# Kernel tuning notes

Hardware: AMD Instinct MI355X
Metric: run time of the kernel (lower is better)

Reference implementation:

```python
import jax, jax.numpy as jnp
import numpy as np

N_Q = 8
DIM = 2 ** N_Q          # 256
DEGREE = 3
ANSATZ_LAYERS = 2


def gelu(x):
    return jax.nn.gelu(x, approximate=False)


def layer_norm(x, g, b, eps=1e-5):
    mu = x.mean(-1, keepdims=True)
    v = x.var(-1, keepdims=True)
    return (x - mu) / jnp.sqrt(v + eps) * g + b


def apply_ry(state, theta, w, n):
    # state: (B, 2^n) complex64, theta: (B,) per-element angle
    half = theta * 0.5
    c, s = jnp.cos(half), jnp.sin(half)
    U = jnp.stack([jnp.stack([c, -s], -1), jnp.stack([s, c], -1)], -2).astype(state.dtype)
    L, R = 2 ** w, 2 ** (n - 1 - w)
    st = state.reshape(-1, L, 2, R)
    st = jnp.einsum('bij,bljr->blir', U, st)
    return st.reshape(state.shape)


def apply_crx(state, theta, c, t, n):
    # controlled-RX(theta), control wire c, target wire t (batched angles)
    half = theta * 0.5
    cs = jnp.cos(half).astype(state.dtype)
    ms = (-1j) * jnp.sin(half).astype(state.dtype)
    Rx = jnp.stack([jnp.stack([cs, ms], -1), jnp.stack([ms, cs], -1)], -2)  # (B,2,2)
    a, b = min(c, t), max(c, t)
    A, M, R = 2 ** a, 2 ** (b - a - 1), 2 ** (n - 1 - b)
    st = state.reshape(-1, A, 2, M, 2, R)
    if c < t:
        sub = st[:, :, 1]                              # control bit = 1 slice, (B,A,M,2,R)
        sub = jnp.einsum('bij,bamjr->bamir', Rx, sub)
        st = st.at[:, :, 1].set(sub)
    else:
        sub = st[:, :, :, :, 1]                        # (B,A,2,M,R)
        sub = jnp.einsum('bij,bajmr->baimr', Rx, sub)
        st = st.at[:, :, :, :, 1].set(sub)
    return st.reshape(state.shape)


def sim14(state, params, n, layers):
    # Sim et al. 2019 circuit 14: RY layer, CRX ring, RY layer, reversed CRX ring (4n params/layer)
    idx = 0
    for _ in range(layers):
        for q in range(n):
            state = apply_ry(state, params[:, idx + q], q, n)
        idx += n
        for q in range(n):
            state = apply_crx(state, params[:, idx + q], q, (q + 1) % n, n)
        idx += n
        for q in range(n):
            state = apply_ry(state, params[:, idx + q], q, n)
        idx += n
        for q in range(n):
            state = apply_crx(state, params[:, idx + q], q, (q - 1) % n, n)
        idx += n
    return state


def pauli_expvals(psi, n):
    # [<X_0..X_{n-1}>, <Y_0..>, <Z_0..>] for batched pure states psi: (B, 2^n)
    xs, ys, zs = [], [], []
    for w in range(n):
        L, R = 2 ** w, 2 ** (n - 1 - w)
        s = psi.reshape(-1, L, 2, R)
        s0, s1 = s[:, :, 0], s[:, :, 1]
        cross = (jnp.conj(s0) * s1).sum((1, 2))
        xs.append(2.0 * jnp.real(cross))
        ys.append(2.0 * jnp.imag(cross))
        zs.append((jnp.abs(s0) ** 2 - jnp.abs(s1) ** 2).sum((1, 2)))
    return jnp.stack(xs + ys + zs, axis=1).astype(jnp.float32)


def dwsep_conv(x, dw_w, dw_b, pw_w, pw_b, gn_g, gn_b, dilation):
    # depthwise-separable conv1d + GroupNorm(8) + GELU; x: (B, C, T)
    k = dw_w.shape[-1]
    pad = (k - 1) * dilation // 2
    y = jax.lax.conv_general_dilated(
        x, dw_w, window_strides=(1,), padding=[(pad, pad)], rhs_dilation=(dilation,),
        feature_group_count=x.shape[1], dimension_numbers=('NCH', 'OIH', 'NCH'))
    y = y + dw_b[None, :, None]
    y = jnp.einsum('oc,bct->bot', pw_w, y) + pw_b[None, :, None]
    B, C, T = y.shape
    g = y.reshape(B, 8, C // 8, T)
    mu = g.mean((2, 3), keepdims=True)
    var = g.var((2, 3), keepdims=True)
    y = ((g - mu) / jnp.sqrt(var + 1e-5)).reshape(B, C, T)
    return gelu(y * gn_g[None, :, None] + gn_b[None, :, None])


def setup_inputs() -> dict:
    key = jax.random.key(0)
    ks = iter(jax.random.split(key, 64))
    rn = lambda *s: jax.random.normal(next(ks), s, jnp.float32) * 0.05
    ru = lambda *s: jax.random.uniform(next(ks), s, dtype=jnp.float32)
    inp = dict(
        x=jax.random.normal(next(ks), (16, 363, 180), jnp.float32),
        net_w=rn(12, 15, 8), net_b=rn(12, 8),
        dwa_w=rn(96, 1, 7), dwa_b=rn(96), pwa_w=rn(96, 96), pwa_b=rn(96),
        gna_g=jnp.ones(96, jnp.float32), gna_b=jnp.zeros(96, jnp.float32),
        dwb_w=rn(96, 1, 7), dwb_b=rn(96), pwb_w=rn(96, 96), pwb_b=rn(96),
        gnb_g=jnp.ones(96, jnp.float32), gnb_b=jnp.zeros(96, jnp.float32),
        dwc_w=rn(96, 1, 7), dwc_b=rn(96), pwc_w=rn(96, 96), pwc_b=rn(96),
        gnc_g=jnp.ones(96, jnp.float32), gnc_b=jnp.zeros(96, jnp.float32),
        merge_w=rn(288, 128), merge_b=rn(128),
        merge_ln_g=jnp.ones(128, jnp.float32), merge_ln_b=jnp.zeros(128, jnp.float32),
        qproj_w=rn(128, 64), qproj_b=rn(64),
        poly_coeffs=ru(4), qff_params=ru(32),
        mix_re=ru(363), mix_im=ru(363),
        qout_w=rn(24, 128), qout_b=rn(128),
        fc_w=rn(78, 64), fc_b=rn(64),
        fus1_w=rn(192, 128), fus1_b=rn(128),
        fus_ln_g=jnp.ones(128, jnp.float32), fus_ln_b=jnp.zeros(128, jnp.float32),
        fus2_w=rn(128, 64), fus2_b=rn(64),
    )
    return inp


def reference(x, net_w, net_b, dwa_w, dwa_b, pwa_w, pwa_b, gna_g, gna_b,
              dwb_w, dwb_b, pwb_w, pwb_b, gnb_g, gnb_b,
              dwc_w, dwc_b, pwc_w, pwc_b, gnc_g, gnc_b,
              merge_w, merge_b, merge_ln_g, merge_ln_b,
              qproj_w, qproj_b, poly_coeffs, qff_params, mix_re, mix_im,
              qout_w, qout_b, fc_w, fc_b,
              fus1_w, fus1_b, fus_ln_g, fus_ln_b, fus2_w, fus2_b):
    B, T, C = x.shape
    # --- network projection: 12 contiguous networks of 15 ROIs -> d_net=8 each ---
    h = jnp.einsum('btki,kid->btkd', x.reshape(B, T, 12, 15), net_w) + net_b
    h = gelu(h).reshape(B, T, 96)
    # --- multiscale depthwise-separable convs ---
    ht = h.transpose(0, 2, 1)  # (B,96,T)
    a = dwsep_conv(ht, dwa_w, dwa_b, pwa_w, pwa_b, gna_g, gna_b, 1)
    b = dwsep_conv(ht, dwb_w, dwb_b, pwb_w, pwb_b, gnb_g, gnb_b, 4)
    c = dwsep_conv(ht, dwc_w, dwc_b, pwc_w, pwc_b, gnc_g, gnc_b, 16)
    cat = jnp.concatenate([a, b, c], axis=1).transpose(0, 2, 1)  # (B,T,288)
    h = gelu(layer_norm(cat @ merge_w + merge_b, merge_ln_g, merge_ln_b))  # (B,T,128)
    # --- QSVT quantum temporal mixing ---
    tp = jax.nn.sigmoid(h @ qproj_w + qproj_b) * (2.0 * np.pi)  # (B,T,64) rotation angles
    tp = tp.reshape(B * T, -1)
    base = jnp.zeros((B * T, DIM), jnp.complex64).at[:, 0].set(1.0)
    pc = poly_coeffs.astype(jnp.complex64)
    state = base
    acc = pc[0] * base
    for d in range(1, DEGREE + 1):
        state = sim14(state, tp, N_Q, ANSATZ_LAYERS)
        acc = acc + pc[d] * state
    acc = acc.reshape(B, T, DIM)
    mix = (mix_re + 1j * mix_im).astype(jnp.complex64)[:T]
    mixed = jnp.einsum('t,btd->bd', mix, acc)           # temporal mixing
    norm = jnp.linalg.norm(mixed, axis=1, keepdims=True)
    psi = mixed / (norm + 1e-9)
    psi = sim14(psi, jnp.broadcast_to(qff_params[None, :], (B, qff_params.shape[0])), N_Q, 1)
    exps = pauli_expvals(psi, N_Q)                      # (B,24)
    temporal = exps @ qout_w + qout_b                   # (B,128)
    # --- FC fingerprint ---
    xm = x - x.mean(1, keepdims=True)
    std = jnp.maximum(jnp.std(x, axis=1, keepdims=True, ddof=1), 1e-8)
    xn = xm / std
    corr = jnp.einsum('btc,btd->bcd', xn, xn) / (T - 1)
    bm = corr.reshape(B, 12, 15, 12, 15).mean((2, 4))   # (B,12,12) network-block means
    iu0, iu1 = jnp.triu_indices(12)
    fc_vec = bm[:, iu0, iu1]                            # (B,78)
    fc = gelu(fc_vec @ fc_w + fc_b)                     # (B,64)
    # --- fusion ---
    fused = jnp.concatenate([temporal, fc], axis=1)
    out = gelu(layer_norm(fused @ fus1_w + fus1_b, fus_ln_g, fus_ln_b)) @ fus2_w + fus2_b
    return out  # (B,64)
```

## Files before the change

kernel.cpp:

```cpp
#include <hip/hip_runtime.h>
#include <math.h>

#define NB 16
#define NT 363
#define NC 180
#define SZF 557568
#define NROW 5808

__device__ __forceinline__ float gelu_f(float x) {
  return 0.5f * x * (1.0f + erff(x * 0.7071067811865475244f));
}


template<int CTRL>
__device__ __forceinline__ float dppf(float x) {
  return __int_as_float(__builtin_amdgcn_update_dpp(
      0, __float_as_int(x), CTRL, 0xF, 0xF, true));
}

template<int LB>
__device__ __forceinline__ float lx(float x) {
  if constexpr (LB == 0) return dppf<0xB1>(x);
  else if constexpr (LB == 1) return dppf<0x4E>(x);
  else if constexpr (LB == 2) return __shfl_xor(x, 4);
  else if constexpr (LB == 3) return __shfl_xor(x, 8);
  else return __shfl_xor(x, 16);
}

template<int P>
__device__ __forceinline__ void ry_local8(float* re, float* im, float c, float s) {
#pragma unroll
  for (int j = 0; j < 8; ++j) {
    if ((j & (1 << P)) == 0) {
      int k = j | (1 << P);
      float r0 = re[j], i0 = im[j], r1 = re[k], i1 = im[k];
      re[j] = fmaf(c, r0, -s * r1); im[j] = fmaf(c, i0, -s * i1);
      re[k] = fmaf(s, r0,  c * r1); im[k] = fmaf(s, i0,  c * i1);
    }
  }
}

template<int LB>
__device__ __forceinline__ void ry_lane8(float* re, float* im, float c, float s, int lane) {
  float sg = (lane & (1 << LB)) ? s : -s;
#pragma unroll
  for (int j = 0; j < 8; ++j) {
    float br = lx<LB>(re[j]);
    float bi = lx<LB>(im[j]);
    re[j] = fmaf(c, re[j], sg * br);
    im[j] = fmaf(c, im[j], sg * bi);
  }
}

template<int Q, int P>
__device__ __forceinline__ void crx_ll8(float* re, float* im, float cs, float sn) {
#pragma unroll
  for (int j = 0; j < 8; ++j) {
    if ((j & (1 << Q)) && !(j & (1 << P))) {
      int k = j | (1 << P);
      float r0 = re[j], i0 = im[j], r1 = re[k], i1 = im[k];
      re[j] = fmaf(cs, r0,  sn * i1); im[j] = fmaf(cs, i0, -sn * r1);
      re[k] = fmaf(cs, r1,  sn * i0); im[k] = fmaf(cs, i1, -sn * r0);
    }
  }
}

template<int LBQ, int P>
__device__ __forceinline__ void crx_nl8(float* re, float* im, float cs, float sn, int lane) {
  if (lane & (1 << LBQ)) {
#pragma unroll
    for (int j = 0; j < 8; ++j) {
      if ((j & (1 << P)) == 0) {
        int k = j | (1 << P);
        float r0 = re[j], i0 = im[j], r1 = re[k], i1 = im[k];
        re[j] = fmaf(cs, r0,  sn * i1); im[j] = fmaf(cs, i0, -sn * r1);
        re[k] = fmaf(cs, r1,  sn * i0); im[k] = fmaf(cs, i1, -sn * r0);
      }
    }
  }
}

template<int Q, int LBP>
__device__ __forceinline__ void crx_ln8(float* re, float* im, float cs, float sn) {
#pragma unroll
  for (int j = 0; j < 8; ++j) {
    if (j & (1 << Q)) {
      float br = lx<LBP>(re[j]);
      float bi = lx<LBP>(im[j]);
      re[j] = fmaf(cs, re[j],  sn * bi);
      im[j] = fmaf(cs, im[j], -sn * br);
    }
  }
}

template<int LBQ, int LBP>
__device__ __forceinline__ void crx_nn8(float* re, float* im, float cs, float sn, int lane) {
  bool ctl = (lane & (1 << LBQ)) != 0;
#pragma unroll
  for (int j = 0; j < 8; ++j) {
    float br = lx<LBP>(re[j]);
    float bi = lx<LBP>(im[j]);
    if (ctl) {
      re[j] = fmaf(cs, re[j],  sn * bi);
      im[j] = fmaf(cs, im[j], -sn * br);
    }
  }
}

__device__ __forceinline__ void qlayer8(float* re, float* im,
                                        const float2* ang, int lane) {
  float2 a;
  a = ang[0];  ry_lane8<4>(re, im, a.x, a.y, lane);
  a = ang[1];  ry_lane8<3>(re, im, a.x, a.y, lane);
  a = ang[2];  ry_lane8<2>(re, im, a.x, a.y, lane);
  a = ang[3];  ry_lane8<1>(re, im, a.x, a.y, lane);
  a = ang[4];  ry_lane8<0>(re, im, a.x, a.y, lane);
  a = ang[5];  ry_local8<2>(re, im, a.x, a.y);
  a = ang[6];  ry_local8<1>(re, im, a.x, a.y);
  a = ang[7];  ry_local8<0>(re, im, a.x, a.y);
  a = ang[8];  crx_nn8<4, 3>(re, im, a.x, a.y, lane);
  a = ang[9];  crx_nn8<3, 2>(re, im, a.x, a.y, lane);
  a = ang[10]; crx_nn8<2, 1>(re, im, a.x, a.y, lane);
  a = ang[11]; crx_nn8<1, 0>(re, im, a.x, a.y, lane);
  a = ang[12]; crx_nl8<0, 2>(re, im, a.x, a.y, lane);
  a = ang[13]; crx_ll8<2, 1>(re, im, a.x, a.y);
  a = ang[14]; crx_ll8<1, 0>(re, im, a.x, a.y);
  a = ang[15]; crx_ln8<0, 4>(re, im, a.x, a.y);
  a = ang[16]; ry_lane8<4>(re, im, a.x, a.y, lane);
  a = ang[17]; ry_lane8<3>(re, im, a.x, a.y, lane);
  a = ang[18]; ry_lane8<2>(re, im, a.x, a.y, lane);
  a = ang[19]; ry_lane8<1>(re, im, a.x, a.y, lane);
  a = ang[20]; ry_lane8<0>(re, im, a.x, a.y, lane);
  a = ang[21]; ry_local8<2>(re, im, a.x, a.y);
  a = ang[22]; ry_local8<1>(re, im, a.x, a.y);
  a = ang[23]; ry_local8<0>(re, im, a.x, a.y);
  a = ang[24]; crx_nl8<4, 0>(re, im, a.x, a.y, lane);
  a = ang[25]; crx_nn8<3, 4>(re, im, a.x, a.y, lane);
  a = ang[26]; crx_nn8<2, 3>(re, im, a.x, a.y, lane);
  a = ang[27]; crx_nn8<1, 2>(re, im, a.x, a.y, lane);
  a = ang[28]; crx_nn8<0, 1>(re, im, a.x, a.y, lane);
  a = ang[29]; crx_ln8<2, 0>(re, im, a.x, a.y);
  a = ang[30]; crx_ll8<1, 2>(re, im, a.x, a.y);
  a = ang[31]; crx_ll8<0, 1>(re, im, a.x, a.y);
}

template<int P>
__device__ __forceinline__ void ryg(float* re, float* im, float c, float s, int lane) {
  if constexpr (P >= 2) {
    constexpr int mask = 1 << (P - 2);
    float sg = ((lane >> (P - 2)) & 1) ? s : -s;
#pragma unroll
    for (int j = 0; j < 4; ++j) {
      float br = __shfl_xor(re[j], mask);
      float bi = __shfl_xor(im[j], mask);
      re[j] = fmaf(c, re[j], sg * br);
      im[j] = fmaf(c, im[j], sg * bi);
    }
  } else {
#pragma unroll
    for (int k = 0; k < 2; ++k) {
      const int a = (P == 0) ? 2 * k : k;
      const int b = (P == 0) ? a + 1 : a + 2;
      float r0 = re[a], i0 = im[a], r1 = re[b], i1 = im[b];
      re[a] = fmaf(c, r0, -s * r1); im[a] = fmaf(c, i0, -s * i1);
      re[b] = fmaf(s, r0,  c * r1); im[b] = fmaf(s, i0,  c * i1);
    }
  }
}

template<int PC, int PT>
__device__ __forceinline__ void crxg(float* re, float* im, float cs, float sn, int lane) {
  if constexpr (PT >= 2) {
    constexpr int mask = 1 << (PT - 2);
#pragma unroll
    for (int j = 0; j < 4; ++j) {
      float br = __shfl_xor(re[j], mask);
      float bi = __shfl_xor(im[j], mask);
      bool ctrl;
      if constexpr (PC >= 2) ctrl = ((lane >> (PC - 2)) & 1) != 0;
      else                   ctrl = ((j >> PC) & 1) != 0;
      if (ctrl) {
        float nr = fmaf(cs, re[j],  sn * bi);
        float ni = fmaf(cs, im[j], -sn * br);
        re[j] = nr; im[j] = ni;
      }
    }
  } else {
#pragma unroll
    for (int k = 0; k < 2; ++k) {
      const int a = (PT == 0) ? 2 * k : k;
      const int b = (PT == 0) ? a + 1 : a + 2;
      bool ctrl;
      if constexpr (PC >= 2) ctrl = ((lane >> (PC - 2)) & 1) != 0;
      else                   ctrl = ((a >> PC) & 1) != 0;
      if (ctrl) {
        float r0 = re[a], i0 = im[a], r1 = re[b], i1 = im[b];
// ... 34 lines not shown
    int z = i / 56, r = i % 56, d = r / 7, k = r % 7;
    const float* w = (z == 0) ? wa : ((z == 1) ? wb : wc);
    wL[z][d][k] = w[(kg * 8 + d) * 7 + k];
  }
  for (int i = tid; i < 24; i += 256) {
    int z = i / 8, d = i % 8;
    const float* bias = (z == 0) ? ba : ((z == 1) ? bb : bc);
    bL[z][d] = bias[kg * 8 + d];
  }
  for (int i = tid; i < NT * 15; i += 256) {
    int t = i / 15, u = i % 15;
    xs[i] = x[((size_t)b * NT + t) * NC + kg * 15 + u];
  }
  __syncthreads();
  for (int i = tid; i < 8 * NT; i += 256) {
    int t = i % NT, d = i / NT;
    float acc2 = nbL[d];
#pragma unroll
    for (int u = 0; u < 15; ++u) acc2 = fmaf(xs[t * 15 + u], nwL[u * 8 + d], acc2);
    hrow[d][t] = gelu_f(acc2);
  }
  __syncthreads();
  for (int i = tid; i < 8 * NT; i += 256) {
    int t = i % NT, d = i / NT;
    int c = kg * 8 + d;
    float a0 = bL[0][d], a1 = bL[1][d], a2 = bL[2][d];
#pragma unroll
    for (int k = 0; k < 7; ++k) {
      int i1 = t + (k - 3);
      int i4 = t + (k - 3) * 4;
      int i16 = t + (k - 3) * 16;
      if (i1 >= 0 && i1 < NT)  a0 = fmaf(hrow[d][i1],  wL[0][d][k], a0);
      if (i4 >= 0 && i4 < NT)  a1 = fmaf(hrow[d][i4],  wL[1][d][k], a1);
      if (i16 >= 0 && i16 < NT) a2 = fmaf(hrow[d][i16], wL[2][d][k], a2);
    }
    size_t base = ((size_t)b * 96 + c) * NT + t;
    y1base[base] = a0;
    y1base[SZF + base] = a1;
    y1base[2 * SZF + base] = a2;
  }
}

__global__ __launch_bounds__(256) void k_pw(const float* __restrict__ y1base,
    const float* __restrict__ wA, const float* __restrict__ wB, const float* __restrict__ wC,
    const float* __restrict__ bA, const float* __restrict__ bB, const float* __restrict__ bC,
    float* __restrict__ y2base) {
  int b = blockIdx.x, tile = blockIdx.y, z = blockIdx.z, tid = threadIdx.x;
  const float* pw_w = (z == 0) ? wA : ((z == 1) ? wB : wC);
  const float* pw_b = (z == 0) ? bA : ((z == 1) ? bB : bC);
  const float* y1 = y1base + (size_t)z * SZF;
  float* y2 = y2base + (size_t)z * SZF;
  int t0 = tile * 64;
  __shared__ float y1t[96 * 64];
  __shared__ float pwL[96 * 97];
  for (int i = tid; i < 96 * 96; i += 256) {
    int o = i / 96, cc = i % 96;
    pwL[o * 97 + cc] = pw_w[i];
  }
  for (int i = tid; i < 96 * 64; i += 256) {
    int cc = i >> 6, t = i & 63;
    int tt = t0 + t;
    y1t[i] = (tt < NT) ? y1[(b * 96 + cc) * NT + tt] : 0.0f;
  }
  __syncthreads();
  int o16 = tid >> 4, t4 = (tid & 15) * 4;
  for (int pass = 0; pass < 6; ++pass) {
    int o = pass * 16 + o16;
    float bias = pw_b[o];
    float a0 = bias, a1 = bias, a2 = bias, a3 = bias;
    const float* wrow = &pwL[o * 97];
#pragma unroll 4
    for (int cc = 0; cc < 96; ++cc) {
      const float4 vy = *reinterpret_cast<const float4*>(&y1t[cc * 64 + t4]);
      float w = wrow[cc];
      a0 = fmaf(w, vy.x, a0); a1 = fmaf(w, vy.y, a1);
      a2 = fmaf(w, vy.z, a2); a3 = fmaf(w, vy.w, a3);
    }
    int base = (b * 96 + o) * NT;
    int t = t0 + t4;
    if (t + 3 < NT) {
      y2[base + t] = a0; y2[base + t + 1] = a1; y2[base + t + 2] = a2; y2[base + t + 3] = a3;
    } else {
      if (t < NT) y2[base + t] = a0;
      if (t + 1 < NT) y2[base + t + 1] = a1;
      if (t + 2 < NT) y2[base + t + 2] = a2;
      if (t + 3 < NT) y2[base + t + 3] = a3;
    }
  }
}

__global__ __launch_bounds__(256) void k_gnstat(const float* __restrict__ y2base,
                                                float* __restrict__ muG,
                                                float* __restrict__ rsG) {
  int b = blockIdx.x, g = blockIdx.y, z = blockIdx.z, tid = threadIdx.x;
  __shared__ float red[256];
  const float* base = y2base + (size_t)z * SZF + (b * 96 + g * 12) * NT;
  float s = 0;
  for (int i = tid; i < 12 * NT; i += 256) s += base[i];
  red[tid] = s; __syncthreads();
  for (int st = 128; st > 0; st >>= 1) { if (tid < st) red[tid] += red[tid + st]; __syncthreads(); }
  float mu = red[0] / 4356.0f;
  __syncthreads();
  float q = 0;
  for (int i = tid; i < 12 * NT; i += 256) { float d = base[i] - mu; q = fmaf(d, d, q); }
  red[tid] = q; __syncthreads();
  for (int st = 128; st > 0; st >>= 1) { if (tid < st) red[tid] += red[tid + st]; __syncthreads(); }
  if (tid == 0) {
    float var = red[0] / 4356.0f;
    muG[(z * NB + b) * 8 + g] = mu;
    rsG[(z * NB + b) * 8 + g] = rsqrtf(var + 1e-5f);
  }
}

__global__ __launch_bounds__(256) void k_gnapply(const float* __restrict__ y2base,
    const float* __restrict__ muG, const float* __restrict__ rsG,
    const float* __restrict__ gA, const float* __restrict__ gB, const float* __restrict__ gC,
    const float* __restrict__ bA, const float* __restrict__ bB, const float* __restrict__ bC,
    float* __restrict__ cat) {
  int b = blockIdx.x, tile = blockIdx.y, z = blockIdx.z, tid = threadIdx.x;
  const float* gng = (z == 0) ? gA : ((z == 1) ? gB : gC);
  const float* gnb = (z == 0) ? bA : ((z == 1) ? bB : bC);
  const float* y2 = y2base + (size_t)z * SZF;
  int t0 = tile * 64;
  __shared__ float yL[96 * 65];
  __shared__ float muL[8], rsL[8];
  if (tid < 8) { muL[tid] = muG[(z * NB + b) * 8 + tid]; rsL[tid] = rsG[(z * NB + b) * 8 + tid]; }
  for (int i = tid; i < 96 * 64; i += 256) {
    int cc = i >> 6, t = i & 63;
    int tt = t0 + t;
    yL[cc * 65 + t] = (tt < NT) ? y2[(b * 96 + cc) * NT + tt] : 0.0f;
  }
  __syncthreads();
  for (int i = tid; i < 64 * 96; i += 256) {
    int tt = i / 96, cc = i % 96;
    int t = t0 + tt;
    if (t < NT) {
      int g = cc / 12;
      float v = (yL[cc * 65 + tt] - muL[g]) * rsL[g] * gng[cc] + gnb[cc];
      cat[(b * NT + t) * 288 + z * 96 + cc] = gelu_f(v);
    }
  }
}

__global__ __launch_bounds__(256) void k_merge(const float* __restrict__ cat,
    const float* __restrict__ mw, const float* __restrict__ mb,
    const float* __restrict__ lng, const float* __restrict__ lnb,
    const float* __restrict__ qw, const float* __restrict__ qb,
    float2* __restrict__ angG) {
  int blk = blockIdx.x, tid = threadIdx.x;
  __shared__ float catL[8][288];
  __shared__ float vL[8][129];
  __shared__ float hL[8][129];
  __shared__ float muS[8], rsS[8];
  for (int i = tid; i < 8 * 288; i += 256) {
    int r = i / 288, k = i % 288;
    catL[r][k] = cat[(blk * 8 + r) * 288 + k];
  }
  __syncthreads();
  int jj = tid & 127, rg = tid >> 7;
  float bias = mb[jj];
  float acc[4] = {bias, bias, bias, bias};
  for (int k = 0; k < 288; ++k) {
    float w = mw[k * 128 + jj];
#pragma unroll
    for (int r = 0; r < 4; ++r) acc[r] = fmaf(catL[rg * 4 + r][k], w, acc[r]);
  }
#pragma unroll
  for (int r = 0; r < 4; ++r) vL[rg * 4 + r][jj] = acc[r];
  __syncthreads();
  if (tid < 8) {
    float s = 0;
    for (int k = 0; k < 128; ++k) s += vL[tid][k];
    float mu = s / 128.0f;
    float q = 0;
    for (int k = 0; k < 128; ++k) { float d = vL[tid][k] - mu; q = fmaf(d, d, q); }
    muS[tid] = mu;
    rsS[tid] = rsqrtf(q / 128.0f + 1e-5f);
  }
  __syncthreads();
  float g = lng[jj], bb2 = lnb[jj];
#pragma unroll
  for (int r = 0; r < 4; ++r) {
    int row = rg * 4 + r;
    float h = (acc[r] - muS[row]) * rsS[row] * g + bb2;
    hL[row][jj] = gelu_f(h);
  }
  __syncthreads();
  int o = tid & 63;
  int r0 = (tid >> 6) * 2;
  for (int rr = 0; rr < 2; ++rr) {
    int row = r0 + rr;
    float u = qb[o];
    for (int k = 0; k < 128; ++k) u = fmaf(hL[row][k], qw[k * 64 + o], u);
    float tp = 6.2831853071795864769f / (1.0f + expf(-u));
    float hf = tp * 0.5f;
    int grow = blk * 8 + row;
    angG[grow * 64 + o] = make_float2(cosf(hf), sinf(hf));
  }
}

struct CorrSM { float mu[180]; float inv[180]; float S[NT * 12]; float fcv[78]; };
union QSM { float2 ang[8][66]; CorrSM c; };

__global__ __launch_bounds__(256) void k_quantum(const float2* __restrict__ angG,
                                                 const float* __restrict__ pc4,
                                                 float* __restrict__ accG,
                                                 const float* __restrict__ x,
                                                 const float* __restrict__ fcw,
                                                 const float* __restrict__ fcb,
                                                 float* __restrict__ fusedG) {
  __shared__ QSM sm;
  int tid = threadIdx.x;
  if (blockIdx.x < NROW / 8) {
    const int lane = tid & 63;
    const int wave = tid >> 6;
    const int ll = lane & 31;
    const int rowB = wave * 2 + (lane >> 5);
    const int row0 = blockIdx.x * 8;
    for (int i = tid; i < 512; i += 256) {
      int r = i >> 6, cidx = i & 63;
      sm.ang[r][cidx] = angG[(size_t)(row0 + r) * 64 + cidx];
    }
    __syncthreads();
    float p0 = pc4[0], p1 = pc4[1], p2 = pc4[2], p3 = pc4[3];
    float re[8], im[8];
#pragma unroll
    for (int j = 0; j < 8; ++j) { re[j] = 0.0f; im[j] = 0.0f; }
    if (ll == 0) re[0] = p3;
    const float2* ang = &sm.ang[rowB][0];
    for (int rep = 0; rep < 3; ++rep) {
      qlayer8(re, im, ang, lane);
      qlayer8(re, im, ang + 32, lane);
      float pc = (rep == 0) ? p2 : (rep == 1) ? p1 : p0;
      if (ll == 0) re[0] += pc;
    }
    int row = row0 + rowB;
    float4* dst = reinterpret_cast<float4*>(accG + ((size_t)row * 256 + ll * 8) * 2);
#pragma unroll
    for (int h = 0; h < 4; ++h)
      dst[h] = make_float4(re[2 * h], im[2 * h], re[2 * h + 1], im[2 * h + 1]);
  } else {
    int b = blockIdx.x - NROW / 8;
    if (tid < 180) {
      float s = 0;
      const float* px = x + (size_t)b * NT * NC + tid;
      for (int t = 0; t < NT; ++t) s += px[t * NC];
      float mu = s / 363.0f;
      float q = 0;
      for (int t = 0; t < NT; ++t) { float d = px[t * NC] - mu; q = fmaf(d, d, q); }
      float sd = sqrtf(q / 362.0f);
      sd = fmaxf(sd, 1e-8f);
      sm.c.mu[tid] = mu; sm.c.inv[tid] = 1.0f / sd;
    }
    __syncthreads();
    for (int t = tid; t < NT; t += 256) {
      const float* px = x + (size_t)(b * NT + t) * NC;
#pragma unroll
      for (int i = 0; i < 12; ++i) {
        float s = 0;
#pragma unroll
        for (int u = 0; u < 15; ++u) {
          int cidx = i * 15 + u;
          s += (px[cidx] - sm.c.mu[cidx]) * sm.c.inv[cidx];
        }
        sm.c.S[t * 12 + i] = s;
      }
    }
    __syncthreads();
    if (tid < 78) {
      int i = 0, rem = tid;
      while (rem >= 12 - i) { rem -= 12 - i; ++i; }
      int j = i + rem;
      float acc = 0;
      for (int t = 0; t < NT; ++t) acc = fmaf(sm.c.S[t * 12 + i], sm.c.S[t * 12 + j], acc);
      sm.c.fcv[tid] = acc * (1.0f / (225.0f * 362.0f));
    }
    __syncthreads();
    if (tid < 64) {
      float v = fcb[tid];
#pragma unroll
      for (int k = 0; k < 78; ++k) v = fmaf(sm.c.fcv[k], fcw[k * 64 + tid], v);
      fusedG[b * 192 + 128 + tid] = gelu_f(v);
    }
  }
}

__global__ __launch_bounds__(256) void k_mix1(const float* __restrict__ accG,
                                              const float* __restrict__ mr,
                                              const float* __restrict__ mi,
                                              float* __restrict__ part) {
  int b = blockIdx.x, ch = blockIdx.y, d = threadIdx.x;
  int t0 = ch * 33;
  float sr = 0, si = 0;
  for (int i = 0; i < 33; ++i) {
    int t = t0 + i;
    const float2 a = *reinterpret_cast<const float2*>(accG + (size_t)((b * NT + t) * 256 + d) * 2);
    float m_r = mr[t], m_i = mi[t];
    sr = fmaf(m_r, a.x, fmaf(-m_i, a.y, sr));
    si = fmaf(m_r, a.y, fmaf(m_i, a.x, si));
  }
  float2* o = reinterpret_cast<float2*>(part + (size_t)((b * 11 + ch) * 256 + d) * 2);
  *o = make_float2(sr, si);
}

__global__ __launch_bounds__(256) void k_tail(const float* __restrict__ part,
    const float* __restrict__ qff,
    const float* __restrict__ qout_w, const float* __restrict__ qout_b,
    const float* __restrict__ fusedG,
    const float* __restrict__ w1, const float* __restrict__ b1,
    const float* __restrict__ lng, const float* __restrict__ lnb,
    const float* __restrict__ w2, const float* __restrict__ b2,
    float* __restrict__ out) {
  int b = blockIdx.x, tid = threadIdx.x;
  __shared__ float psiL[256][2];
  __shared__ float red[256];
  __shared__ float qcL[32], qsL[32], exps[24];
  __shared__ float tL[128], cL[64], hL[128];
  {
    float sr = 0, si = 0;
    for (int ch = 0; ch < 11; ++ch) {
      const float2 a = *reinterpret_cast<const float2*>(part + (size_t)((b * 11 + ch) * 256 + tid) * 2);
      sr += a.x; si += a.y;
    }
    psiL[tid][0] = sr; psiL[tid][1] = si;
    red[tid] = sr * sr + si * si;
  }
  if (tid < 32) { float h = qff[tid] * 0.5f; qcL[tid] = cosf(h); qsL[tid] = sinf(h); }
  __syncthreads();
  for (int s2 = 128; s2 > 0; s2 >>= 1) { if (tid < s2) red[tid] += red[tid + s2]; __syncthreads(); }
  float inv = 1.0f / (sqrtf(red[0]) + 1e-9f);
  __syncthreads();
  if (tid < 64) {
    int lane = tid;
    float re[4], im[4];
#pragma unroll
    for (int j = 0; j < 4; ++j) {
      re[j] = psiL[lane * 4 + j][0] * inv;
      im[j] = psiL[lane * 4 + j][1] * inv;
    }
    sim14_layer(re, im, qcL, qsL, lane);
#pragma unroll
    for (int j = 0; j < 4; ++j) { psiL[lane * 4 + j][0] = re[j]; psiL[lane * 4 + j][1] = im[j]; }
  }
  __syncthreads();
  if (tid < 64) {
    int lane = tid;
    for (int w = 0; w < 8; ++w) {
      int p = 7 - w;
      float cr = 0, ci = 0, z = 0;
#pragma unroll
      for (int k = 0; k < 2; ++k) {
        int pr = lane + k * 64;
        int lowmask = (1 << p) - 1;
        int i0 = ((pr >> p) << (p + 1)) | (pr & lowmask);
        int i1 = i0 | (1 << p);
        float r0 = psiL[i0][0], I0 = psiL[i0][1], r1 = psiL[i1][0], I1 = psiL[i1][1];
        cr += r0 * r1 + I0 * I1;
        ci += r0 * I1 - I0 * r1;
        z += r0 * r0 + I0 * I0 - r1 * r1 - I1 * I1;
      }
      for (int off = 32; off > 0; off >>= 1) {
        cr += __shfl_down(cr, off);
        ci += __shfl_down(ci, off);
        z  += __shfl_down(z, off);
      }
      if (lane == 0) { exps[w] = 2.0f * cr; exps[8 + w] = 2.0f * ci; exps[16 + w] = z; }
    }
  }
  __syncthreads();
  if (tid < 128) {
    float v = qout_b[tid];
#pragma unroll
    for (int k = 0; k < 24; ++k) v = fmaf(exps[k], qout_w[k * 128 + tid], v);
    tL[tid] = v;
  } else if (tid < 192) {
// ... 27 lines not shown

extern "C" void kernel_launch(void* const* d_in, const int* in_sizes, int n_in,
                              void* d_out, int out_size, void* d_ws, size_t ws_size,
                              hipStream_t stream) {
  const float* x       = (const float*)d_in[0];
  const float* net_w   = (const float*)d_in[1];
  const float* net_b   = (const float*)d_in[2];
  const float* dwa_w   = (const float*)d_in[3];
  const float* dwa_b   = (const float*)d_in[4];
  const float* pwa_w   = (const float*)d_in[5];
  const float* pwa_b   = (const float*)d_in[6];
  const float* gna_g   = (const float*)d_in[7];
  const float* gna_b   = (const float*)d_in[8];
  const float* dwb_w   = (const float*)d_in[9];
  const float* dwb_b   = (const float*)d_in[10];
  const float* pwb_w   = (const float*)d_in[11];
  const float* pwb_b   = (const float*)d_in[12];
  const float* gnb_g   = (const float*)d_in[13];
  const float* gnb_b   = (const float*)d_in[14];
  const float* dwc_w   = (const float*)d_in[15];
  const float* dwc_b   = (const float*)d_in[16];
  const float* pwc_w   = (const float*)d_in[17];
  const float* pwc_b   = (const float*)d_in[18];
  const float* gnc_g   = (const float*)d_in[19];
  const float* gnc_b   = (const float*)d_in[20];
  const float* merge_w = (const float*)d_in[21];
  const float* merge_b = (const float*)d_in[22];
  const float* mlng    = (const float*)d_in[23];
  const float* mlnb    = (const float*)d_in[24];
  const float* qproj_w = (const float*)d_in[25];
  const float* qproj_b = (const float*)d_in[26];
  const float* poly    = (const float*)d_in[27];
  const float* qff     = (const float*)d_in[28];
  const float* mix_re  = (const float*)d_in[29];
  const float* mix_im  = (const float*)d_in[30];
  const float* qout_w  = (const float*)d_in[31];
  const float* qout_b  = (const float*)d_in[32];
  const float* fc_w    = (const float*)d_in[33];
  const float* fc_b    = (const float*)d_in[34];
  const float* fus1_w  = (const float*)d_in[35];
  const float* fus1_b  = (const float*)d_in[36];
  const float* flng    = (const float*)d_in[37];
  const float* flnb    = (const float*)d_in[38];
  const float* fus2_w  = (const float*)d_in[39];
  const float* fus2_b  = (const float*)d_in[40];
  float* out = (float*)d_out;

  float* W = (float*)d_ws;
  float* y1b_  = W;
  float* cat   = W;
  float* y2b_  = W + 3 * (size_t)SZF;
  float* acc   = W;
  float2* angG = (float2*)(W + 6 * (size_t)SZF);
  float* muG   = W + 6 * (size_t)SZF + 743424;
  float* rsG   = muG + 512;
  float* part  = rsG + 512;
  float* fused = part + 90112;

  k_emdw<<<dim3(NB, 12), 256, 0, stream>>>(x, net_w, net_b,
      dwa_w, dwa_b, dwb_w, dwb_b, dwc_w, dwc_b, y1b_);
  k_pw<<<dim3(NB, 6, 3), 256, 0, stream>>>(y1b_, pwa_w, pwb_w, pwc_w, pwa_b, pwb_b, pwc_b, y2b_);
  k_gnstat<<<dim3(NB, 8, 3), 256, 0, stream>>>(y2b_, muG, rsG);
  k_gnapply<<<dim3(NB, 6, 3), 256, 0, stream>>>(y2b_, muG, rsG,
      gna_g, gnb_g, gnc_g, gna_b, gnb_b, gnc_b, cat);
  k_merge<<<(NB * NT) / 8, 256, 0, stream>>>(cat, merge_w, merge_b, mlng, mlnb,
                                             qproj_w, qproj_b, angG);
  k_quantum<<<NROW / 8 + NB, 256, 0, stream>>>(angG, poly, acc, x, fc_w, fc_b, fused);
  k_mix1<<<dim3(NB, 11), 256, 0, stream>>>(acc, mix_re, mix_im, part);
  k_tail<<<NB, 256, 0, stream>>>(part, qff, qout_w, qout_b, fused,
                                 fus1_w, fus1_b, flng, flnb, fus2_w, fus2_b, out);
}
```

Before: 335.1 us.

## Restructure kernel pipeline: fuse GN stats, move FC into merge, widen quantum state per lane

Merges the group-norm statistics and apply kernels into one kernel that recomputes stats per tile using single-pass sum and sum-of-squares. The FC fingerprint branch moves from the quantum kernel to the merge kernel. The quantum simulation now uses 16 amplitudes per lane with 16 lanes per row in 64-thread blocks, replacing 8 amplitudes on 32 lanes. The temporal mixing kernel is folded into the tail kernel, which now loops over all timesteps serially in only 16 blocks. It also vectorizes weight and activation loads in the pointwise and merge matmuls and changes shared padding. Launch count drops, but the GN stats are recomputed redundantly in each tile, and the tail loses parallelism.

```diff
diff --git a/kernel.cpp b/kernel.cpp
--- a/kernel.cpp
+++ b/kernel.cpp
@@ -23,14 +23,13 @@
   if constexpr (LB == 0) return dppf<0xB1>(x);
   else if constexpr (LB == 1) return dppf<0x4E>(x);
   else if constexpr (LB == 2) return __shfl_xor(x, 4);
-  else if constexpr (LB == 3) return __shfl_xor(x, 8);
-  else return __shfl_xor(x, 16);
+  else return __shfl_xor(x, 8);
 }
 
 template<int P>
-__device__ __forceinline__ void ry_local8(float* re, float* im, float c, float s) {
-#pragma unroll
-  for (int j = 0; j < 8; ++j) {
+__device__ __forceinline__ void ry_local(float* re, float* im, float c, float s) {
+#pragma unroll
+  for (int j = 0; j < 16; ++j) {
     if ((j & (1 << P)) == 0) {
       int k = j | (1 << P);
       float r0 = re[j], i0 = im[j], r1 = re[k], i1 = im[k];
@@ -41,10 +40,10 @@
 }
 
 template<int LB>
-__device__ __forceinline__ void ry_lane8(float* re, float* im, float c, float s, int lane) {
+__device__ __forceinline__ void ry_lane(float* re, float* im, float c, float s, int lane) {
   float sg = (lane & (1 << LB)) ? s : -s;
 #pragma unroll
-  for (int j = 0; j < 8; ++j) {
+  for (int j = 0; j < 16; ++j) {
     float br = lx<LB>(re[j]);
     float bi = lx<LB>(im[j]);
     re[j] = fmaf(c, re[j], sg * br);
@@ -53,9 +52,9 @@
 }
 
 template<int Q, int P>
-__device__ __forceinline__ void crx_ll8(float* re, float* im, float cs, float sn) {
-#pragma unroll
-  for (int j = 0; j < 8; ++j) {
+__device__ __forceinline__ void crx_ll(float* re, float* im, float cs, float sn) {
+#pragma unroll
+  for (int j = 0; j < 16; ++j) {
     if ((j & (1 << Q)) && !(j & (1 << P))) {
       int k = j | (1 << P);
       float r0 = re[j], i0 = im[j], r1 = re[k], i1 = im[k];
@@ -66,10 +65,10 @@
 }
 
 template<int LBQ, int P>
-__device__ __forceinline__ void crx_nl8(float* re, float* im, float cs, float sn, int lane) {
+__device__ __forceinline__ void crx_nl(float* re, float* im, float cs, float sn, int lane) {
   if (lane & (1 << LBQ)) {
 #pragma unroll
-    for (int j = 0; j < 8; ++j) {
+    for (int j = 0; j < 16; ++j) {
       if ((j & (1 << P)) == 0) {
         int k = j | (1 << P);
         float r0 = re[j], i0 = im[j], r1 = re[k], i1 = im[k];
@@ -81,9 +80,9 @@
 }
 
 template<int Q, int LBP>
-__device__ __forceinline__ void crx_ln8(float* re, float* im, float cs, float sn) {
-#pragma unroll
-  for (int j = 0; j < 8; ++j) {
+__device__ __forceinline__ void crx_ln(float* re, float* im, float cs, float sn) {
+#pragma unroll
+  for (int j = 0; j < 16; ++j) {
     if (j & (1 << Q)) {
       float br = lx<LBP>(re[j]);
       float bi = lx<LBP>(im[j]);
@@ -94,10 +93,10 @@
 }
 
 template<int LBQ, int LBP>
-__device__ __forceinline__ void crx_nn8(float* re, float* im, float cs, float sn, int lane) {
+__device__ __forceinline__ void crx_nn(float* re, float* im, float cs, float sn, int lane) {
   bool ctl = (lane & (1 << LBQ)) != 0;
 #pragma unroll
-  for (int j = 0; j < 8; ++j) {
+  for (int j = 0; j < 16; ++j) {
     float br = lx<LBP>(re[j]);
     float bi = lx<LBP>(im[j]);
     if (ctl) {
@@ -107,41 +106,41 @@
   }
 }
 
-__device__ __forceinline__ void qlayer8(float* re, float* im,
-                                        const float2* ang, int lane) {
+__device__ __forceinline__ void qlayer(float* re, float* im,
+                                       const float2* ang, int lane) {
   float2 a;
-  a = ang[0];  ry_lane8<4>(re, im, a.x, a.y, lane);
-  a = ang[1];  ry_lane8<3>(re, im, a.x, a.y, lane);
-  a = ang[2];  ry_lane8<2>(re, im, a.x, a.y, lane);
-  a = ang[3];  ry_lane8<1>(re, im, a.x, a.y, lane);
-  a = ang[4];  ry_lane8<0>(re, im, a.x, a.y, lane);
-  a = ang[5];  ry_local8<2>(re, im, a.x, a.y);
-  a = ang[6];  ry_local8<1>(re, im, a.x, a.y);
-  a = ang[7];  ry_local8<0>(re, im, a.x, a.y);
-  a = ang[8];  crx_nn8<4, 3>(re, im, a.x, a.y, lane);
-  a = ang[9];  crx_nn8<3, 2>(re, im, a.x, a.y, lane);
-  a = ang[10]; crx_nn8<2, 1>(re, im, a.x, a.y, lane);
-  a = ang[11]; crx_nn8<1, 0>(re, im, a.x, a.y, lane);
-  a = ang[12]; crx_nl8<0, 2>(re, im, a.x, a.y, lane);
-  a = ang[13]; crx_ll8<2, 1>(re, im, a.x, a.y);
-  a = ang[14]; crx_ll8<1, 0>(re, im, a.x, a.y);
-  a = ang[15]; crx_ln8<0, 4>(re, im, a.x, a.y);
-  a = ang[16]; ry_lane8<4>(re, im, a.x, a.y, lane);
-  a = ang[17]; ry_lane8<3>(re, im, a.x, a.y, lane);
-  a = ang[18]; ry_lane8<2>(re, im, a.x, a.y, lane);
-  a = ang[19]; ry_lane8<1>(re, im, a.x, a.y, lane);
-  a = ang[20]; ry_lane8<0>(re, im, a.x, a.y, lane);
-  a = ang[21]; ry_local8<2>(re, im, a.x, a.y);
-  a = ang[22]; ry_local8<1>(re, im, a.x, a.y);
-  a = ang[23]; ry_local8<0>(re, im, a.x, a.y);
-  a = ang[24]; crx_nl8<4, 0>(re, im, a.x, a.y, lane);
-  a = ang[25]; crx_nn8<3, 4>(re, im, a.x, a.y, lane);
-  a = ang[26]; crx_nn8<2, 3>(re, im, a.x, a.y, lane);
-  a = ang[27]; crx_nn8<1, 2>(re, im, a.x, a.y, lane);
-  a = ang[28]; crx_nn8<0, 1>(re, im, a.x, a.y, lane);
-  a = ang[29]; crx_ln8<2, 0>(re, im, a.x, a.y);
-  a = ang[30]; crx_ll8<1, 2>(re, im, a.x, a.y);
-  a = ang[31]; crx_ll8<0, 1>(re, im, a.x, a.y);
+  a = ang[0];  ry_lane<3>(re, im, a.x, a.y, lane);
+  a = ang[1];  ry_lane<2>(re, im, a.x, a.y, lane);
+  a = ang[2];  ry_lane<1>(re, im, a.x, a.y, lane);
+  a = ang[3];  ry_lane<0>(re, im, a.x, a.y, lane);
+  a = ang[4];  ry_local<3>(re, im, a.x, a.y);
+  a = ang[5];  ry_local<2>(re, im, a.x, a.y);
+  a = ang[6];  ry_local<1>(re, im, a.x, a.y);
+  a = ang[7];  ry_local<0>(re, im, a.x, a.y);
+  a = ang[8];  crx_nn<3, 2>(re, im, a.x, a.y, lane);
+  a = ang[9];  crx_nn<2, 1>(re, im, a.x, a.y, lane);
+  a = ang[10]; crx_nn<1, 0>(re, im, a.x, a.y, lane);
+  a = ang[11]; crx_nl<0, 3>(re, im, a.x, a.y, lane);
+  a = ang[12]; crx_ll<3, 2>(re, im, a.x, a.y);
+  a = ang[13]; crx_ll<2, 1>(re, im, a.x, a.y);
+  a = ang[14]; crx_ll<1, 0>(re, im, a.x, a.y);
+  a = ang[15]; crx_ln<0, 3>(re, im, a.x, a.y);
+  a = ang[16]; ry_lane<3>(re, im, a.x, a.y, lane);
+  a = ang[17]; ry_lane<2>(re, im, a.x, a.y, lane);
+  a = ang[18]; ry_lane<1>(re, im, a.x, a.y, lane);
+  a = ang[19]; ry_lane<0>(re, im, a.x, a.y, lane);
+  a = ang[20]; ry_local<3>(re, im, a.x, a.y);
+  a = ang[21]; ry_local<2>(re, im, a.x, a.y);
+  a = ang[22]; ry_local<1>(re, im, a.x, a.y);
+  a = ang[23]; ry_local<0>(re, im, a.x, a.y);
+  a = ang[24]; crx_nl<3, 0>(re, im, a.x, a.y, lane);
+  a = ang[25]; crx_nn<2, 3>(re, im, a.x, a.y, lane);
+  a = ang[26]; crx_nn<1, 2>(re, im, a.x, a.y, lane);
+  a = ang[27]; crx_nn<0, 1>(re, im, a.x, a.y, lane);
+  a = ang[28]; crx_ln<3, 0>(re, im, a.x, a.y);
+  a = ang[29]; crx_ll<2, 3>(re, im, a.x, a.y);
+  a = ang[30]; crx_ll<1, 2>(re, im, a.x, a.y);
+  a = ang[31]; crx_ll<0, 1>(re, im, a.x, a.y);
 }
 
 template<int P>
@@ -282,10 +281,10 @@
   float* y2 = y2base + (size_t)z * SZF;
   int t0 = tile * 64;
   __shared__ float y1t[96 * 64];
-  __shared__ float pwL[96 * 97];
+  __shared__ float pwL[96 * 100];
   for (int i = tid; i < 96 * 96; i += 256) {
     int o = i / 96, cc = i % 96;
-    pwL[o * 97 + cc] = pw_w[i];
+    pwL[o * 100 + cc] = pw_w[i];
   }
   for (int i = tid; i < 96 * 64; i += 256) {
     int cc = i >> 6, t = i & 63;
@@ -298,13 +297,17 @@
     int o = pass * 16 + o16;
     float bias = pw_b[o];
     float a0 = bias, a1 = bias, a2 = bias, a3 = bias;
-    const float* wrow = &pwL[o * 97];
-#pragma unroll 4
-    for (int cc = 0; cc < 96; ++cc) {
-      const float4 vy = *reinterpret_cast<const float4*>(&y1t[cc * 64 + t4]);
-      float w = wrow[cc];
-      a0 = fmaf(w, vy.x, a0); a1 = fmaf(w, vy.y, a1);
-      a2 = fmaf(w, vy.z, a2); a3 = fmaf(w, vy.w, a3);
+    const float* wrow = &pwL[o * 100];
+    for (int cc4 = 0; cc4 < 24; ++cc4) {
+      const float4 w4 = *reinterpret_cast<const float4*>(&wrow[cc4 * 4]);
+#pragma unroll
+      for (int e = 0; e < 4; ++e) {
+        int cc = cc4 * 4 + e;
+        const float4 vy = *reinterpret_cast<const float4*>(&y1t[cc * 64 + t4]);
+        float w = (e == 0) ? w4.x : (e == 1) ? w4.y : (e == 2) ? w4.z : w4.w;
+        a0 = fmaf(w, vy.x, a0); a1 = fmaf(w, vy.y, a1);
+        a2 = fmaf(w, vy.z, a2); a3 = fmaf(w, vy.w, a3);
+      }
     }
     int base = (b * 96 + o) * NT;
     int t = t0 + t4;
@@ -319,46 +322,40 @@
   }
 }
 
-__global__ __launch_bounds__(256) void k_gnstat(const float* __restrict__ y2base,
-                                                float* __restrict__ muG,
-                                                float* __restrict__ rsG) {
-  int b = blockIdx.x, g = blockIdx.y, z = blockIdx.z, tid = threadIdx.x;
-  __shared__ float red[256];
-  const float* base = y2base + (size_t)z * SZF + (b * 96 + g * 12) * NT;
-  float s = 0;
-  for (int i = tid; i < 12 * NT; i += 256) s += base[i];
-  red[tid] = s; __syncthreads();
-  for (int st = 128; st > 0; st >>= 1) { if (tid < st) red[tid] += red[tid + st]; __syncthreads(); }
-  float mu = red[0] / 4356.0f;
-  __syncthreads();
-  float q = 0;
-  for (int i = tid; i < 12 * NT; i += 256) { float d = base[i] - mu; q = fmaf(d, d, q); }
-  red[tid] = q; __syncthreads();
-  for (int st = 128; st > 0; st >>= 1) { if (tid < st) red[tid] += red[tid + st]; __syncthreads(); }
-  if (tid == 0) {
-    float var = red[0] / 4356.0f;
-    muG[(z * NB + b) * 8 + g] = mu;
-    rsG[(z * NB + b) * 8 + g] = rsqrtf(var + 1e-5f);
-  }
-}
-
-__global__ __launch_bounds__(256) void k_gnapply(const float* __restrict__ y2base,
-    const float* __restrict__ muG, const float* __restrict__ rsG,
+__global__ __launch_bounds__(256) void k_gn(const float* __restrict__ y2base,
     const float* __restrict__ gA, const float* __restrict__ gB, const float* __restrict__ gC,
     const float* __restrict__ bA, const float* __restrict__ bB, const float* __restrict__ bC,
     float* __restrict__ cat) {
   int b = blockIdx.x, tile = blockIdx.y, z = blockIdx.z, tid = threadIdx.x;
   const float* gng = (z == 0) ? gA : ((z == 1) ? gB : gC);
   const float* gnb = (z == 0) ? bA : ((z == 1) ? bB : bC);
-  const float* y2 = y2base + (size_t)z * SZF;
+  const float* y2 = y2base + (size_t)z * SZF + (size_t)b * 96 * NT;
+  __shared__ float redS[256], redQ[256];
+  __shared__ float muL[8], rsL[8];
+  __shared__ float yL[96 * 65];
+  for (int g = 0; g < 8; ++g) {
+    const float* gb = y2 + g * 12 * NT;
+    float s = 0, q = 0;
+    for (int i = tid; i < 12 * NT; i += 256) { float v = gb[i]; s += v; q = fmaf(v, v, q); }
+    redS[tid] = s; redQ[tid] = q;
+    __syncthreads();
+    for (int st = 128; st > 0; st >>= 1) {
+      if (tid < st) { redS[tid] += redS[tid + st]; redQ[tid] += redQ[tid + st]; }
+      __syncthreads();
+    }
+    if (tid == 0) {
+      float mu = redS[0] / 4356.0f;
+      float var = redQ[0] / 4356.0f - mu * mu;
+      muL[g] = mu;
+      rsL[g] = rsqrtf(fmaxf(var, 0.0f) + 1e-5f);
+    }
+    __syncthreads();
+  }
   int t0 = tile * 64;
-  __shared__ float yL[96 * 65];
-  __shared__ float muL[8], rsL[8];
-  if (tid < 8) { muL[tid] = muG[(z * NB + b) * 8 + tid]; rsL[tid] = rsG[(z * NB + b) * 8 + tid]; }
   for (int i = tid; i < 96 * 64; i += 256) {
     int cc = i >> 6, t = i & 63;
     int tt = t0 + t;
-    yL[cc * 65 + t] = (tt < NT) ? y2[(b * 96 + cc) * NT + tt] : 0.0f;
+    yL[cc * 65 + t] = (tt < NT) ? y2[cc * NT + tt] : 0.0f;
   }
   __syncthreads();
   for (int i = tid; i < 64 * 96; i += 256) {
@@ -367,110 +364,98 @@
     if (t < NT) {
       int g = cc / 12;
       float v = (yL[cc * 65 + tt] - muL[g]) * rsL[g] * gng[cc] + gnb[cc];
-      cat[(b * NT + t) * 288 + z * 96 + cc] = gelu_f(v);
-    }
-  }
-}
+      cat[((size_t)b * NT + t) * 288 + z * 96 + cc] = gelu_f(v);
+    }
+  }
+}
+
+struct CorrSM { float mu[180]; float inv[180]; float S[NT * 12]; float fcv[78]; };
+struct MergeSM {
+  float catL[8][288];
+  float vL[8][132];
+  float hL[8][132];
+  float muS[8], rsS[8];
+};
+union MCSM { MergeSM m; CorrSM c; };
 
 __global__ __launch_bounds__(256) void k_merge(const float* __restrict__ cat,
     const float* __restrict__ mw, const float* __restrict__ mb,
     const float* __restrict__ lng, const float* __restrict__ lnb,
     const float* __restrict__ qw, const float* __restrict__ qb,
-    float2* __restrict__ angG) {
-  int blk = blockIdx.x, tid = threadIdx.x;
-  __shared__ float catL[8][288];
-  __shared__ float vL[8][129];
-  __shared__ float hL[8][129];
-  __shared__ float muS[8], rsS[8];
-  for (int i = tid; i < 8 * 288; i += 256) {
-    int r = i / 288, k = i % 288;
-    catL[r][k] = cat[(blk * 8 + r) * 288 + k];
-  }
-  __syncthreads();
-  int jj = tid & 127, rg = tid >> 7;
-  float bias = mb[jj];
-  float acc[4] = {bias, bias, bias, bias};
-  for (int k = 0; k < 288; ++k) {
-    float w = mw[k * 128 + jj];
-#pragma unroll
-    for (int r = 0; r < 4; ++r) acc[r] = fmaf(catL[rg * 4 + r][k], w, acc[r]);
-  }
-#pragma unroll
-  for (int r = 0; r < 4; ++r) vL[rg * 4 + r][jj] = acc[r];
-  __syncthreads();
-  if (tid < 8) {
-    float s = 0;
-    for (int k = 0; k < 128; ++k) s += vL[tid][k];
-    float mu = s / 128.0f;
-    float q = 0;
-    for (int k = 0; k < 128; ++k) { float d = vL[tid][k] - mu; q = fmaf(d, d, q); }
-    muS[tid] = mu;
-    rsS[tid] = rsqrtf(q / 128.0f + 1e-5f);
-  }
-  __syncthreads();
-  float g = lng[jj], bb2 = lnb[jj];
-#pragma unroll
-  for (int r = 0; r < 4; ++r) {
-    int row = rg * 4 + r;
-    float h = (acc[r] - muS[row]) * rsS[row] * g + bb2;
-    hL[row][jj] = gelu_f(h);
-  }
-  __syncthreads();
-  int o = tid & 63;
-  int r0 = (tid >> 6) * 2;
-  for (int rr = 0; rr < 2; ++rr) {
-    int row = r0 + rr;
-    float u = qb[o];
-    for (int k = 0; k < 128; ++k) u = fmaf(hL[row][k], qw[k * 64 + o], u);
-    float tp = 6.2831853071795864769f / (1.0f + expf(-u));
-    float hf = tp * 0.5f;
-    int grow = blk * 8 + row;
-    angG[grow * 64 + o] = make_float2(cosf(hf), sinf(hf));
-  }
-}
-
-struct CorrSM { float mu[180]; float inv[180]; float S[NT * 12]; float fcv[78]; };
-union QSM { float2 ang[8][66]; CorrSM c; };
-
-__global__ __launch_bounds__(256) void k_quantum(const float2* __restrict__ angG,
-                                                 const float* __restrict__ pc4,
-                                                 float* __restrict__ accG,
-                                                 const float* __restrict__ x,
-                                                 const float* __restrict__ fcw,
-                                                 const float* __restrict__ fcb,
-                                                 float* __restrict__ fusedG) {
-  __shared__ QSM sm;
+    float2* __restrict__ angG,
+    const float* __restrict__ x,
+    const float* __restrict__ fcw, const float* __restrict__ fcb,
+    float* __restrict__ fusedG) {
+  __shared__ MCSM sm;
   int tid = threadIdx.x;
-  if (blockIdx.x < NROW / 8) {
-    const int lane = tid & 63;
-    const int wave = tid >> 6;
-    const int ll = lane & 31;
-    const int rowB = wave * 2 + (lane >> 5);
-    const int row0 = blockIdx.x * 8;
-    for (int i = tid; i < 512; i += 256) {
-      int r = i >> 6, cidx = i & 63;
-      sm.ang[r][cidx] = angG[(size_t)(row0 + r) * 64 + cidx];
-    }
-    __syncthreads();
-    float p0 = pc4[0], p1 = pc4[1], p2 = pc4[2], p3 = pc4[3];
-    float re[8], im[8];
-#pragma unroll
-    for (int j = 0; j < 8; ++j) { re[j] = 0.0f; im[j] = 0.0f; }
-    if (ll == 0) re[0] = p3;
-    const float2* ang = &sm.ang[rowB][0];
-    for (int rep = 0; rep < 3; ++rep) {
-      qlayer8(re, im, ang, lane);
-      qlayer8(re, im, ang + 32, lane);
-      float pc = (rep == 0) ? p2 : (rep == 1) ? p1 : p0;
-      if (ll == 0) re[0] += pc;
-    }
-    int row = row0 + rowB;
-    float4* dst = reinterpret_cast<float4*>(accG + ((size_t)row * 256 + ll * 8) * 2);
-#pragma unroll
-    for (int h = 0; h < 4; ++h)
-      dst[h] = make_float4(re[2 * h], im[2 * h], re[2 * h + 1], im[2 * h + 1]);
+  if (blockIdx.x < 726) {
+    int blk = blockIdx.x;
+    for (int i = tid; i < 8 * 288; i += 256) {
+      int r = i / 288, k = i % 288;
+      sm.m.catL[r][k] = cat[((size_t)blk * 8 + r) * 288 + k];
+    }
+    __syncthreads();
+    int jj = tid & 127, rg = tid >> 7;
+    float bias = mb[jj];
+    float acc[4] = {bias, bias, bias, bias};
+    {
+      const float4* c0 = reinterpret_cast<const float4*>(&sm.m.catL[rg * 4 + 0][0]);
+      const float4* c1 = reinterpret_cast<const float4*>(&sm.m.catL[rg * 4 + 1][0]);
+      const float4* c2 = reinterpret_cast<const float4*>(&sm.m.catL[rg * 4 + 2][0]);
+      const float4* c3 = reinterpret_cast<const float4*>(&sm.m.catL[rg * 4 + 3][0]);
+      for (int k4 = 0; k4 < 72; ++k4) {
+        float w0 = mw[(k4 * 4 + 0) * 128 + jj];
+        float w1 = mw[(k4 * 4 + 1) * 128 + jj];
+        float w2 = mw[(k4 * 4 + 2) * 128 + jj];
+        float w3 = mw[(k4 * 4 + 3) * 128 + jj];
+        float4 v0 = c0[k4], v1 = c1[k4], v2 = c2[k4], v3 = c3[k4];
+        acc[0] = fmaf(v0.x, w0, fmaf(v0.y, w1, fmaf(v0.z, w2, fmaf(v0.w, w3, acc[0]))));
+        acc[1] = fmaf(v1.x, w0, fmaf(v1.y, w1, fmaf(v1.z, w2, fmaf(v1.w, w3, acc[1]))));
+        acc[2] = fmaf(v2.x, w0, fmaf(v2.y, w1, fmaf(v2.z, w2, fmaf(v2.w, w3, acc[2]))));
+        acc[3] = fmaf(v3.x, w0, fmaf(v3.y, w1, fmaf(v3.z, w2, fmaf(v3.w, w3, acc[3]))));
+      }
+    }
+#pragma unroll
+    for (int r = 0; r < 4; ++r) sm.m.vL[rg * 4 + r][jj] = acc[r];
+    __syncthreads();
+    if (tid < 8) {
+      float s = 0;
+      for (int k = 0; k < 128; ++k) s += sm.m.vL[tid][k];
+      float mu = s / 128.0f;
+      float q = 0;
+      for (int k = 0; k < 128; ++k) { float d = sm.m.vL[tid][k] - mu; q = fmaf(d, d, q); }
+      sm.m.muS[tid] = mu;
+      sm.m.rsS[tid] = rsqrtf(q / 128.0f + 1e-5f);
+    }
+    __syncthreads();
+    float g = lng[jj], bb2 = lnb[jj];
+#pragma unroll
+    for (int r = 0; r < 4; ++r) {
+      int row = rg * 4 + r;
+      float h = (acc[r] - sm.m.muS[row]) * sm.m.rsS[row] * g + bb2;
+      sm.m.hL[row][jj] = gelu_f(h);
+    }
+    __syncthreads();
+    int o = tid & 63;
+    int r0 = (tid >> 6) * 2;
+    for (int rr = 0; rr < 2; ++rr) {
+      int row = r0 + rr;
+      float u = qb[o];
+      const float4* h4 = reinterpret_cast<const float4*>(&sm.m.hL[row][0]);
+      for (int k4 = 0; k4 < 32; ++k4) {
+        float4 hv = h4[k4];
+        u = fmaf(hv.x, qw[(k4 * 4 + 0) * 64 + o],
+            fmaf(hv.y, qw[(k4 * 4 + 1) * 64 + o],
+            fmaf(hv.z, qw[(k4 * 4 + 2) * 64 + o],
+            fmaf(hv.w, qw[(k4 * 4 + 3) * 64 + o], u))));
+      }
+      float tp = 6.2831853071795864769f / (1.0f + expf(-u));
+      float hf = tp * 0.5f;
+      int grow = blk * 8 + row;
+      angG[(size_t)grow * 64 + o] = make_float2(cosf(hf), sinf(hf));
+    }
   } else {
-    int b = blockIdx.x - NROW / 8;
+    int b = blockIdx.x - 726;
     if (tid < 180) {
       float s = 0;
       const float* px = x + (size_t)b * NT * NC + tid;
@@ -515,25 +500,39 @@
   }
 }
 
-__global__ __launch_bounds__(256) void k_mix1(const float* __restrict__ accG,
-                                              const float* __restrict__ mr,
-                                              const float* __restrict__ mi,
-                                              float* __restrict__ part) {
-  int b = blockIdx.x, ch = blockIdx.y, d = threadIdx.x;
-  int t0 = ch * 33;
-  float sr = 0, si = 0;
-  for (int i = 0; i < 33; ++i) {
-    int t = t0 + i;
-    const float2 a = *reinterpret_cast<const float2*>(accG + (size_t)((b * NT + t) * 256 + d) * 2);
-    float m_r = mr[t], m_i = mi[t];
-    sr = fmaf(m_r, a.x, fmaf(-m_i, a.y, sr));
-    si = fmaf(m_r, a.y, fmaf(m_i, a.x, si));
-  }
-  float2* o = reinterpret_cast<float2*>(part + (size_t)((b * 11 + ch) * 256 + d) * 2);
-  *o = make_float2(sr, si);
-}
-
-__global__ __launch_bounds__(256) void k_tail(const float* __restrict__ part,
+__global__ __launch_bounds__(64) void k_quantum(const float2* __restrict__ angG,
+                                                const float* __restrict__ pc4,
+                                                float* __restrict__ accG) {
+  const int lane = threadIdx.x;
+  const int g = lane >> 4;
+  const int ll = lane & 15;
+  const int row0 = blockIdx.x * 4;
+  __shared__ float2 angL[4][66];
+#pragma unroll
+  for (int q = 0; q < 4; ++q)
+    angL[q][lane] = angG[(size_t)(row0 + q) * 64 + lane];
+  __syncthreads();
+  float p0 = pc4[0], p1 = pc4[1], p2 = pc4[2], p3 = pc4[3];
+  float re[16], im[16];
+#pragma unroll
+  for (int j = 0; j < 16; ++j) { re[j] = 0.0f; im[j] = 0.0f; }
+  if (ll == 0) re[0] = p3;
+  const float2* ang = &angL[g][0];
+  for (int rep = 0; rep < 3; ++rep) {
+    qlayer(re, im, ang, lane);
+    qlayer(re, im, ang + 32, lane);
+    float pc = (rep == 0) ? p2 : (rep == 1) ? p1 : p0;
+    if (ll == 0) re[0] += pc;
+  }
+  int row = row0 + g;
+  float4* dst = reinterpret_cast<float4*>(accG + ((size_t)row * 256 + ll * 16) * 2);
+#pragma unroll
+  for (int h = 0; h < 8; ++h)
+    dst[h] = make_float4(re[2 * h], im[2 * h], re[2 * h + 1], im[2 * h + 1]);
+}
+
+__global__ __launch_bounds__(256) void k_tail(const float* __restrict__ accG,
+    const float* __restrict__ mr, const float* __restrict__ mi,
     const float* __restrict__ qff,
     const float* __restrict__ qout_w, const float* __restrict__ qout_b,
     const float* __restrict__ fusedG,
@@ -547,10 +546,14 @@
   __shared__ float qcL[32], qsL[32], exps[24];
   __shared__ float tL[128], cL[64], hL[128];
   {
+    const float2* av = reinterpret_cast<const float2*>(accG) + (size_t)b * NT * 256 + tid;
     float sr = 0, si = 0;
-    for (int ch = 0; ch < 11; ++ch) {
-      const float2 a = *reinterpret_cast<const float2*>(part + (size_t)((b * 11 + ch) * 256 + tid) * 2);
-      sr += a.x; si += a.y;
+#pragma unroll 3
+    for (int t = 0; t < NT; ++t) {
+      float2 a = av[(size_t)t * 256];
+      float m_r = mr[t], m_i = mi[t];
+      sr = fmaf(m_r, a.x, fmaf(-m_i, a.y, sr));
+      si = fmaf(m_r, a.y, fmaf(m_i, a.x, si));
     }
     psiL[tid][0] = sr; psiL[tid][1] = si;
     red[tid] = sr * sr + si * si;
@@ -684,21 +687,16 @@
   float* y2b_  = W + 3 * (size_t)SZF;
   float* acc   = W;
   float2* angG = (float2*)(W + 6 * (size_t)SZF);
-  float* muG   = W + 6 * (size_t)SZF + 743424;
-  float* rsG   = muG + 512;
-  float* part  = rsG + 512;
-  float* fused = part + 90112;
+  float* fused = W + 6 * (size_t)SZF + 743424;
 
   k_emdw<<<dim3(NB, 12), 256, 0, stream>>>(x, net_w, net_b,
       dwa_w, dwa_b, dwb_w, dwb_b, dwc_w, dwc_b, y1b_);
   k_pw<<<dim3(NB, 6, 3), 256, 0, stream>>>(y1b_, pwa_w, pwb_w, pwc_w, pwa_b, pwb_b, pwc_b, y2b_);
-  k_gnstat<<<dim3(NB, 8, 3), 256, 0, stream>>>(y2b_, muG, rsG);
-  k_gnapply<<<dim3(NB, 6, 3), 256, 0, stream>>>(y2b_, muG, rsG,
+  k_gn<<<dim3(NB, 6, 3), 256, 0, stream>>>(y2b_,
       gna_g, gnb_g, gnc_g, gna_b, gnb_b, gnc_b, cat);
-  k_merge<<<(NB * NT) / 8, 256, 0, stream>>>(cat, merge_w, merge_b, mlng, mlnb,
-                                             qproj_w, qproj_b, angG);
-  k_quantum<<<NROW / 8 + NB, 256, 0, stream>>>(angG, poly, acc, x, fc_w, fc_b, fused);
-  k_mix1<<<dim3(NB, 11), 256, 0, stream>>>(acc, mix_re, mix_im, part);
-  k_tail<<<NB, 256, 0, stream>>>(part, qff, qout_w, qout_b, fused,
+  k_merge<<<726 + NB, 256, 0, stream>>>(cat, merge_w, merge_b, mlng, mlnb,
+      qproj_w, qproj_b, angG, x, fc_w, fc_b, fused);
+  k_quantum<<<NROW / 4, 64, 0, stream>>>(angG, poly, acc);
+  k_tail<<<NB, 256, 0, stream>>>(acc, mix_re, mix_im, qff, qout_w, qout_b, fused,
                                  fus1_w, fus1_b, flng, flnb, fus2_w, fus2_b, out);
 }
```

Measured after the change: 538.9 us. 1.61x slower.
